# Performance work log

Hardware: AMD Instinct MI355X
Metric: run time of the kernel (lower is better)

Reference implementation:

```python
import jax, jax.numpy as jnp
import numpy as np

BLOCK = 8
ITERS = 8
EPS = 1e-5
SHAPE = (64, 64, 64)
BATCH = 16


def overlapping_blocks(x, bs):
    # x: [B, M, N, K] -> per-block copies with a 1-cell zero-padded halo:
    # [B, nm, nn, nk, bs+2, bs+2, bs+2]
    B, M, N, K = x.shape
    p = jnp.pad(x, ((0, 0), (1, 1), (1, 1), (1, 1)))

    def gather(a, axis, n, size):
        idx = (jnp.arange(n)[:, None] * bs + jnp.arange(size)[None, :]).reshape(-1)
        a = jnp.take(a, idx, axis=axis)
        return a.reshape(a.shape[:axis] + (n, size) + a.shape[axis + 1:])

    nm, nn, nk = M // bs, N // bs, K // bs
    p = gather(p, 1, nm, bs + 2)   # [B, nm, P, N+2, K+2]
    p = gather(p, 3, nn, bs + 2)   # [B, nm, P, nn, P, K+2]
    p = gather(p, 5, nk, bs + 2)   # [B, nm, P, nn, P, nk, P]
    return p.transpose(0, 1, 3, 5, 2, 4, 6)


def param_blocks(w, bs):
    # [..., M, N, K] -> [..., nm, nn, nk, bs, bs, bs] (non-overlapping)
    lead = w.shape[:-3]
    M, N, K = w.shape[-3:]
    w = w.reshape(*lead, M // bs, bs, N // bs, bs, K // bs, bs)
    nl = len(lead)
    perm = tuple(range(nl)) + (nl, nl + 2, nl + 4, nl + 1, nl + 3, nl + 5)
    return w.transpose(perm)


def gridnet_step(weight, bias, residual_scale, x, inner_iterations, block_size,
                 eps=EPS, normalize=True):
    bs = block_size
    blocks = overlapping_blocks(x, bs)            # [B, nm, nn, nk, P, P, P]
    wb = param_blocks(weight, bs)                 # [27, nm, nn, nk, bs, bs, bs]
    bb = param_blocks(bias, bs)                   # [nm, nn, nk, bs, bs, bs]
    rb = param_blocks(residual_scale, bs)
    inner = (slice(None),) * 4 + (slice(1, -1),) * 3

    for _ in range(inner_iterations):
        if normalize:
            mean = blocks.mean(axis=(-3, -2, -1), keepdims=True)
            var = blocks.var(axis=(-3, -2, -1), keepdims=True)
            normed = (blocks - mean) / jnp.sqrt(var + eps)
        else:
            normed = blocks
        dot = jnp.zeros_like(blocks[inner])
        tap = 0
        for dx in range(3):
            for dy in range(3):
                for dz in range(3):
                    nb = normed[..., dx:dx + bs, dy:dy + bs, dz:dz + bs]
                    dot = dot + nb * wb[tap]
                    tap += 1
        out = blocks[inner] + rb * jax.nn.silu(dot + bb)
        # only interior cells update; halo stays at initial (synced) values
        blocks = blocks.at[inner].set(out)

    y = blocks[inner]                              # [B, nm, nn, nk, bs, bs, bs]
    B, nm, nn, nk = y.shape[:4]
    return y.transpose(0, 1, 4, 2, 5, 3, 6).reshape(B, nm * bs, nn * bs, nk * bs)


def setup_inputs() -> dict:
    key = jax.random.key(0)
    k_w, k_x = jax.random.split(key)
    M, N, K = SHAPE
    weight = jax.random.normal(k_w, (27, M, N, K), dtype=jnp.float32) / np.sqrt(27.0).astype(np.float32)
    bias = jnp.zeros((M, N, K), dtype=jnp.float32)
    residual_scale = jnp.ones((M, N, K), dtype=jnp.float32)
    x = jax.random.normal(k_x, (BATCH, M, N, K), dtype=jnp.float32)
    return {"weight": weight, "bias": bias, "residual_scale": residual_scale, "x": x}


def reference(weight, bias, residual_scale, x):
    return gridnet_step(weight, bias, residual_scale, x, ITERS, BLOCK, EPS, True)
```

## Files before the change

kernel.cpp:

```cpp
#include <hip/hip_runtime.h>

typedef _Float16 h2 __attribute__((ext_vector_type(2)));

#define CSTR 7
#define COLH 14

template <int CTRL>
__device__ __forceinline__ float dpp_stage(float v) {
    int x = __builtin_amdgcn_update_dpp(0, __float_as_int(v), CTRL, 0xf, 0xf, true);
    return v + __int_as_float(x);
}
__device__ __forceinline__ float wave_sum(float v) {
    v = dpp_stage<0x111>(v);
    v = dpp_stage<0x112>(v);
    v = dpp_stage<0x114>(v);
    v = dpp_stage<0x118>(v);
    v = dpp_stage<0x142>(v);
    v = dpp_stage<0x143>(v);
    return v;
}

#define RFL(x) __int_as_float(__builtin_amdgcn_readfirstlane(__float_as_int(x)))

__device__ __forceinline__ h2 mid2(h2 lo, h2 hi) {
    int r = __builtin_amdgcn_alignbit(__builtin_bit_cast(int, hi),
                                      __builtin_bit_cast(int, lo), 16);
    return __builtin_bit_cast(h2, r);
}
__device__ __forceinline__ h2 pkrtz(float a, float b) {
    return __builtin_bit_cast(h2, __builtin_amdgcn_cvt_pkrtz(a, b));
}

#define R27(M) M(0) M(1) M(2) M(3) M(4) M(5) M(6) M(7) M(8) M(9) M(10) M(11) \
    M(12) M(13) M(14) M(15) M(16) M(17) M(18) M(19) M(20) M(21) M(22) M(23)  \
    M(24) M(25) M(26)

#define LOADW(T)                                                               \
    float4 f##T = *(const float4*)(W + ((size_t)(T) << 18) + ofs);             \
    h2 w##T##p = pkrtz(f##T.x, f##T.y);                                        \
    h2 w##T##q = pkrtz(f##T.z, f##T.w);                                        \
    sw0 += f##T.x; sw1 += f##T.y; sw2 += f##T.z; sw3 += f##T.w;

#define COLN(BP, O, T0, T1, T2, D0N, D1N) {                                    \
    h2 d0 = BP[(O)], d1 = BP[(O) + 1], d2 = BP[(O) + 2];                       \
    h2 m0 = mid2(d0, d1), m1 = mid2(d1, d2);                                   \
    D0N = __builtin_elementwise_fma(d0, w##T0##p, D0N);                        \
    D1N = __builtin_elementwise_fma(d1, w##T0##q, D1N);                        \
    D0N = __builtin_elementwise_fma(m0, w##T1##p, D0N);                        \
    D1N = __builtin_elementwise_fma(m1, w##T1##q, D1N);                        \
    D0N = __builtin_elementwise_fma(d1, w##T2##p, D0N);                        \
    D1N = __builtin_elementwise_fma(d2, w##T2##q, D1N); }

#define DOT27(BP, D0N, D1N)                                                    \
    COLN(BP, 0,    0,  1,  2, D0N, D1N)                                        \
    COLN(BP, 7,    3,  4,  5, D0N, D1N)                                        \
    COLN(BP, 14,   6,  7,  8, D0N, D1N)                                        \
    COLN(BP, 70,   9, 10, 11, D0N, D1N)                                        \
    COLN(BP, 77,  12, 13, 14, D0N, D1N)                                        \
    COLN(BP, 84,  15, 16, 17, D0N, D1N)                                        \
    COLN(BP, 140, 18, 19, 20, D0N, D1N)                                        \
    COLN(BP, 147, 21, 22, 23, D0N, D1N)                                        \
    COLN(BP, 154, 24, 25, 26, D0N, D1N)

#define SILU(U) ((U) * __builtin_amdgcn_rcpf(1.f + __expf(-(U))))

#define EPI4(DD0, DD1, SI, QI, HS, HQ, C0, C1, C2, C3, DSTB) {                 \
    float mean = (HS + SI) * inv_n;                                            \
    float istd = rsqrtf((HQ + QI) * inv_n - mean * mean + 1e-5f);              \
    float u0 = ((float)DD0.x - mean * sw0) * istd + bf.x;                      \
    float u1 = ((float)DD0.y - mean * sw1) * istd + bf.y;                      \
    float u2 = ((float)DD1.x - mean * sw2) * istd + bf.z;                      \
    float u3 = ((float)DD1.y - mean * sw3) * istd + bf.w;                      \
    C0 += rf.x * SILU(u0);                                                     \
    C1 += rf.y * SILU(u1);                                                     \
    C2 += rf.z * SILU(u2);                                                     \
    C3 += rf.w * SILU(u3);                                                     \
    DSTB[ipc] = (_Float16)C0;                                                  \
    *(h2*)&DSTB[ipc + 1] = pkrtz(C1, C2);                                      \
    DSTB[ipc + 3] = (_Float16)C3;  }

#define ITERP(BPA, DSTA, BPB, DSTB, RED) {                                     \
    h2 ddA0 = { (_Float16)0.f, (_Float16)0.f };                                \
    h2 ddA1 = ddA0, ddB0 = ddA0, ddB1 = ddA0;                                  \
    DOT27(BPA, ddA0, ddA1)                                                     \
    DOT27(BPB, ddB0, ddB1)                                                     \
    EPI4(ddA0, ddA1, SiA, QiA, halo_sA, halo_qA, cA0, cA1, cA2, cA3, DSTA)     \
    EPI4(ddB0, ddB1, SiB, QiB, halo_sB, halo_qB, cB0, cB1, cB2, cB3, DSTB)     \
    float spA = wave_sum((cA0 + cA1) + (cA2 + cA3));                           \
    float qpA = wave_sum((cA0 * cA0 + cA1 * cA1) + (cA2 * cA2 + cA3 * cA3));   \
    float spB = wave_sum((cB0 + cB1) + (cB2 + cB3));                           \
    float qpB = wave_sum((cB0 * cB0 + cB1 * cB1) + (cB2 * cB2 + cB3 * cB3));   \
    if (lane == 63) { RED[0][wave] = make_float2(spA, qpA);                    \
                      RED[1][wave] = make_float2(spB, qpB); }                  \
    __syncthreads();                                                           \
    SiA = RFL(RED[0][0].x + RED[0][1].x);                                      \
    QiA = RFL(RED[0][0].y + RED[0][1].y);                                      \
    SiB = RFL(RED[1][0].x + RED[1][1].x);                                      \
    QiB = RFL(RED[1][0].y + RED[1][1].y); }

__global__ __launch_bounds__(128)
void gridnet_kernel(const float* __restrict__ W,
                    const float* __restrict__ Bias,
                    const float* __restrict__ Rs,
                    const float* __restrict__ X,
                    float* __restrict__ Y,
                    int n_batch)
{
    __shared__ __align__(16) _Float16 buf[2][2][100 * COLH];
    __shared__ float4 red4[2][2];
    __shared__ float2 redP[2][2][2];

    const int tid = threadIdx.x;
    const int h    = tid & 1;
    const int ly   = (tid >> 1) & 7;
    const int lx   = (tid >> 4) & 7;
    const int wave = tid >> 6;
    const int lane = tid & 63;

    const int np    = n_batch >> 1;
    const int bid   = blockIdx.x;
    const int r     = bid / np;
    const int pb    = bid - r * np;
    const int batch0 = 2 * pb;
    const int gm0 = (r >> 6) << 3;
    const int gn0 = ((r >> 3) & 7) << 3;
    const int gk0 = (r & 7) << 3;

    const float* xb = X + ((size_t)batch0 << 18);

    float sA_all = 0.f, qA_all = 0.f, sA_int = 0.f, qA_int = 0.f;
    float sB_all = 0.f, qB_all = 0.f, sB_int = 0.f, qB_int = 0.f;
    for (int i = tid; i < 1000; i += 128) {
        int ix = i / 100;
        int rem = i - ix * 100;
        int iy = rem / 10;
        int iz = rem - iy * 10;
        int m = gm0 + ix - 1, n = gn0 + iy - 1, k = gk0 + iz - 1;
        float vA = 0.f, vB = 0.f;
        if ((unsigned)m < 64u && (unsigned)n < 64u && (unsigned)k < 64u) {
            const float* p = xb + (m << 12) + (n << 6) + k;
            vA = p[0];
            vB = p[1 << 18];
        }
        _Float16 hA = (_Float16)vA, hB = (_Float16)vB;
        int a = (ix * 10 + iy) * COLH + iz;
        buf[0][0][a] = hA; buf[0][1][a] = hA;
        buf[1][0][a] = hB; buf[1][1][a] = hB;
        float fA = (float)hA, fB = (float)hB;
        sA_all += fA; qA_all += fA * fA;
        sB_all += fB; qB_all += fB * fB;
        bool interior = ((unsigned)(ix - 1) < 8u) & ((unsigned)(iy - 1) < 8u) &
                        ((unsigned)(iz - 1) < 8u);
        if (interior) { sA_int += fA; qA_int += fA * fA;
                        sB_int += fB; qB_int += fB * fB; }
    }

    {
        float a0 = wave_sum(sA_all), a1 = wave_sum(qA_all);
        float a2 = wave_sum(sA_int), a3 = wave_sum(qA_int);
        float b0 = wave_sum(sB_all), b1 = wave_sum(qB_all);
        float b2 = wave_sum(sB_int), b3 = wave_sum(qB_int);
        if (lane == 63) {
            red4[0][wave] = make_float4(a0, a1, a2, a3);
            red4[1][wave] = make_float4(b0, b1, b2, b3);
        }
    }

    const int gm = gm0 + lx, gn = gn0 + ly;
    const size_t ofs = ((size_t)gm << 12) + (gn << 6) + gk0 + 4 * h;
    float sw0 = 0.f, sw1 = 0.f, sw2 = 0.f, sw3 = 0.f;
    R27(LOADW)
    const float4 bf = *(const float4*)(Bias + ofs);
    const float4 rf = *(const float4*)(Rs + ofs);

    __syncthreads();

    float SA = 0.f, QA = 0.f, SiA = 0.f, QiA = 0.f;
    float SB = 0.f, QB = 0.f, SiB = 0.f, QiB = 0.f;
    #pragma unroll
    for (int wv = 0; wv < 2; ++wv) {
        float4 tA = red4[0][wv];
        float4 tB = red4[1][wv];
        SA += tA.x; QA += tA.y; SiA += tA.z; QiA += tA.w;
        SB += tB.x; QB += tB.y; SiB += tB.z; QiB += tB.w;
    }
    const float halo_sA = RFL(SA - SiA), halo_qA = RFL(QA - QiA);
    const float halo_sB = RFL(SB - SiB), halo_qB = RFL(QB - QiB);
    SiA = RFL(SiA); QiA = RFL(QiA);
    SiB = RFL(SiB); QiB = RFL(QiB);

    const int bpD = (lx * 10 + ly) * CSTR + 2 * h;
    const h2* const bpA0 = (const h2*)buf[0][0] + bpD;
    const h2* const bpA1 = (const h2*)buf[0][1] + bpD;
    const h2* const bpB0 = (const h2*)buf[1][0] + bpD;
    const h2* const bpB1 = (const h2*)buf[1][1] + bpD;
    _Float16* const wrA0 = buf[0][0];
    _Float16* const wrA1 = buf[0][1];
    _Float16* const wrB0 = buf[1][0];
    _Float16* const wrB1 = buf[1][1];
    const int ipc = ((lx + 1) * 10 + (ly + 1)) * COLH + 4 * h + 1;
    float cA0 = (float)wrA0[ipc],     cA1 = (float)wrA0[ipc + 1];
    float cA2 = (float)wrA0[ipc + 2], cA3 = (float)wrA0[ipc + 3];
    float cB0 = (float)wrB0[ipc],     cB1 = (float)wrB0[ipc + 1];
    float cB2 = (float)wrB0[ipc + 2], cB3 = (float)wrB0[ipc + 3];

    const float inv_n = 1.0f / 1000.0f;

    #pragma unroll 1
    for (int it = 0; it < 4; ++it) {
        ITERP(bpA0, wrA1, bpB0, wrB1, redP[0])
        ITERP(bpA1, wrA0, bpB1, wrB0, redP[1])
    }

    float* yp = Y + ((size_t)batch0 << 18) + ofs;
    *(float4*)yp = make_float4(cA0, cA1, cA2, cA3);
    *(float4*)(yp + (1 << 18)) = make_float4(cB0, cB1, cB2, cB3);
}

extern "C" void kernel_launch(void* const* d_in, const int* in_sizes, int n_in,
                              void* d_out, int out_size, void* d_ws, size_t ws_size,
                              hipStream_t stream) {
    const float* W = (const float*)d_in[0];
    const float* B = (const float*)d_in[1];
    const float* R = (const float*)d_in[2];
    const float* X = (const float*)d_in[3];
    float* Y = (float*)d_out;

    int n_batch = in_sizes[3] >> 18;
    dim3 grid(512 * (n_batch >> 1)), block(128);
    hipLaunchKernelGGL(gridnet_kernel, grid, block, 0, stream, W, B, R, X, Y, n_batch);
}
```

Before: 153.3 us.

## Park packed fp16 stencil weights in AccVGPRs and interleave the two block dot products

The 54 packed-fp16 weight registers are now stored in accumulation VGPRs with inline v_accvgpr_write and read back just before each column's FMAs. The two blocks' 27-tap dot products are interleaved column by column so each weight read serves both. Launch bounds now request 3 waves per SIMD. The goal is to cut arch VGPR pressure and raise occupancy, at the cost of extra accvgpr read instructions and volatile asm that limits compiler scheduling.

```diff
diff --git a/kernel.cpp b/kernel.cpp
--- a/kernel.cpp
+++ b/kernel.cpp
@@ -36,31 +36,43 @@
     M(24) M(25) M(26)
 
 #define LOADW(T)                                                               \
-    float4 f##T = *(const float4*)(W + ((size_t)(T) << 18) + ofs);             \
-    h2 w##T##p = pkrtz(f##T.x, f##T.y);                                        \
-    h2 w##T##q = pkrtz(f##T.z, f##T.w);                                        \
-    sw0 += f##T.x; sw1 += f##T.y; sw2 += f##T.z; sw3 += f##T.w;
-
-#define COLN(BP, O, T0, T1, T2, D0N, D1N) {                                    \
-    h2 d0 = BP[(O)], d1 = BP[(O) + 1], d2 = BP[(O) + 2];                       \
-    h2 m0 = mid2(d0, d1), m1 = mid2(d1, d2);                                   \
-    D0N = __builtin_elementwise_fma(d0, w##T0##p, D0N);                        \
-    D1N = __builtin_elementwise_fma(d1, w##T0##q, D1N);                        \
-    D0N = __builtin_elementwise_fma(m0, w##T1##p, D0N);                        \
-    D1N = __builtin_elementwise_fma(m1, w##T1##q, D1N);                        \
-    D0N = __builtin_elementwise_fma(d1, w##T2##p, D0N);                        \
-    D1N = __builtin_elementwise_fma(d2, w##T2##q, D1N); }
-
-#define DOT27(BP, D0N, D1N)                                                    \
-    COLN(BP, 0,    0,  1,  2, D0N, D1N)                                        \
-    COLN(BP, 7,    3,  4,  5, D0N, D1N)                                        \
-    COLN(BP, 14,   6,  7,  8, D0N, D1N)                                        \
-    COLN(BP, 70,   9, 10, 11, D0N, D1N)                                        \
-    COLN(BP, 77,  12, 13, 14, D0N, D1N)                                        \
-    COLN(BP, 84,  15, 16, 17, D0N, D1N)                                        \
-    COLN(BP, 140, 18, 19, 20, D0N, D1N)                                        \
-    COLN(BP, 147, 21, 22, 23, D0N, D1N)                                        \
-    COLN(BP, 154, 24, 25, 26, D0N, D1N)
+    int aw##T##p, aw##T##q;                                                    \
+    {                                                                          \
+        const float* wp = W + ((size_t)(T) << 18) + ofs;                       \
+        float4 f = *(const float4*)(wp);                                       \
+        h2 hp = pkrtz(f.x, f.y), hq = pkrtz(f.z, f.w);                         \
+        asm volatile("v_accvgpr_write_b32 %0, %1"                              \
+                     : "=a"(aw##T##p) : "v"(__builtin_bit_cast(int, hp)));     \
+        asm volatile("v_accvgpr_write_b32 %0, %1"                              \
+                     : "=a"(aw##T##q) : "v"(__builtin_bit_cast(int, hq)));     \
+        sw0 += f.x; sw1 += f.y; sw2 += f.z; sw3 += f.w;                        \
+    }
+
+#define AGRD(DST, SRC)                                                         \
+    int _i##DST; asm volatile("v_accvgpr_read_b32 %0, %1"                      \
+                              : "=v"(_i##DST) : "a"(SRC));                     \
+    h2 DST = __builtin_bit_cast(h2, _i##DST);
+
+#define COL2(O, T0, T1, T2) {                                                  \
+    AGRD(wp0, aw##T0##p) AGRD(wq0, aw##T0##q)                                  \
+    AGRD(wp1, aw##T1##p) AGRD(wq1, aw##T1##q)                                  \
+    AGRD(wp2, aw##T2##p) AGRD(wq2, aw##T2##q)                                  \
+    h2 a0 = bpA[(O)], a1 = bpA[(O) + 1], a2 = bpA[(O) + 2];                    \
+    h2 am0 = mid2(a0, a1), am1 = mid2(a1, a2);                                 \
+    ddA0 = __builtin_elementwise_fma(a0,  wp0, ddA0);                          \
+    ddA1 = __builtin_elementwise_fma(a1,  wq0, ddA1);                          \
+    ddA0 = __builtin_elementwise_fma(am0, wp1, ddA0);                          \
+    ddA1 = __builtin_elementwise_fma(am1, wq1, ddA1);                          \
+    ddA0 = __builtin_elementwise_fma(a1,  wp2, ddA0);                          \
+    ddA1 = __builtin_elementwise_fma(a2,  wq2, ddA1);                          \
+    h2 b0 = bpB[(O)], b1 = bpB[(O) + 1], b2 = bpB[(O) + 2];                    \
+    h2 bm0 = mid2(b0, b1), bm1 = mid2(b1, b2);                                 \
+    ddB0 = __builtin_elementwise_fma(b0,  wp0, ddB0);                          \
+    ddB1 = __builtin_elementwise_fma(b1,  wq0, ddB1);                          \
+    ddB0 = __builtin_elementwise_fma(bm0, wp1, ddB0);                          \
+    ddB1 = __builtin_elementwise_fma(bm1, wq1, ddB1);                          \
+    ddB0 = __builtin_elementwise_fma(b1,  wp2, ddB0);                          \
+    ddB1 = __builtin_elementwise_fma(b2,  wq2, ddB1); }
 
 #define SILU(U) ((U) * __builtin_amdgcn_rcpf(1.f + __expf(-(U))))
 
@@ -79,11 +91,20 @@
     *(h2*)&DSTB[ipc + 1] = pkrtz(C1, C2);                                      \
     DSTB[ipc + 3] = (_Float16)C3;  }
 
-#define ITERP(BPA, DSTA, BPB, DSTB, RED) {                                     \
+#define ITERP(BPA_, DSTA, BPB_, DSTB, RED) {                                   \
+    const h2* bpA = BPA_;                                                      \
+    const h2* bpB = BPB_;                                                      \
     h2 ddA0 = { (_Float16)0.f, (_Float16)0.f };                                \
     h2 ddA1 = ddA0, ddB0 = ddA0, ddB1 = ddA0;                                  \
-    DOT27(BPA, ddA0, ddA1)                                                     \
-    DOT27(BPB, ddB0, ddB1)                                                     \
+    COL2(0,    0,  1,  2)                                                      \
+    COL2(7,    3,  4,  5)                                                      \
+    COL2(14,   6,  7,  8)                                                      \
+    COL2(70,   9, 10, 11)                                                      \
+    COL2(77,  12, 13, 14)                                                      \
+    COL2(84,  15, 16, 17)                                                      \
+    COL2(140, 18, 19, 20)                                                      \
+    COL2(147, 21, 22, 23)                                                      \
+    COL2(154, 24, 25, 26)                                                      \
     EPI4(ddA0, ddA1, SiA, QiA, halo_sA, halo_qA, cA0, cA1, cA2, cA3, DSTA)     \
     EPI4(ddB0, ddB1, SiB, QiB, halo_sB, halo_qB, cB0, cB1, cB2, cB3, DSTB)     \
     float spA = wave_sum((cA0 + cA1) + (cA2 + cA3));                           \
@@ -98,7 +119,7 @@
     SiB = RFL(RED[1][0].x + RED[1][1].x);                                      \
     QiB = RFL(RED[1][0].y + RED[1][1].y); }
 
-__global__ __launch_bounds__(128)
+__global__ __launch_bounds__(128, 3)
 void gridnet_kernel(const float* __restrict__ W,
                     const float* __restrict__ Bias,
                     const float* __restrict__ Rs,
```

Measured after the change: 170.1 us. 10.9% more time.
